# Optimization experiments

Hardware: AMD Instinct MI355X
Metric: run time of the kernel (lower is better)

The kernel has to match this reference:

```python
import jax, jax.numpy as jnp
import numpy as np
from jax.ops import segment_sum, segment_max

N = 50000      # nodes
E = 600000     # edges
D_IN = 128     # input_dim
H = 128        # hidden_dim
OUT = 32       # output_dim (classes)
G = 50         # graphs in batch
HEADS = 2


def setup_inputs() -> dict:
    key = jax.random.key(0)
    ks = jax.random.split(key, 16)
    s = 0.05
    inp = {
        "x": jax.random.normal(ks[0], (N, D_IN), jnp.float32),
        "edge_index": jax.random.randint(ks[1], (2, E), 0, N, dtype=jnp.int64),
        "batch": jnp.sort(jax.random.randint(ks[2], (N,), 0, G, dtype=jnp.int64)),
        # GCN layers: weight [in, out] (applied as x @ W), bias [out]
        "W1": jax.random.normal(ks[3], (D_IN, H), jnp.float32) * s,
        "b1": jnp.zeros((H,), jnp.float32),
        "W2": jax.random.normal(ks[4], (H, H), jnp.float32) * s,
        "b2": jnp.zeros((H,), jnp.float32),
        "W3": jax.random.normal(ks[5], (H, H), jnp.float32) * s,
        "b3": jnp.zeros((H,), jnp.float32),
        # GAT: lin weight [H, HEADS*H], attention vecs [HEADS, H], bias [H] (concat=False)
        "gat_W": jax.random.normal(ks[6], (H, HEADS * H), jnp.float32) * s,
        "att_src": jax.random.normal(ks[7], (HEADS, H), jnp.float32) * s,
        "att_dst": jax.random.normal(ks[8], (HEADS, H), jnp.float32) * s,
        "gat_b": jnp.zeros((H,), jnp.float32),
        # MLP head
        "fc1_W": jax.random.normal(ks[9], (H, H), jnp.float32) * s,
        "fc1_b": jnp.zeros((H,), jnp.float32),
        "fc2_W": jax.random.normal(ks[10], (H, OUT), jnp.float32) * s,
        "fc2_b": jnp.zeros((OUT,), jnp.float32),
    }
    return inp


def _add_self_loops(src, dst, n):
    loop = jnp.arange(n, dtype=src.dtype)
    return jnp.concatenate([src, loop]), jnp.concatenate([dst, loop])


def _gcn_conv(x, W, b, src, dst, n):
    # PyG GCNConv: self-loops + symmetric normalization deg^-1/2 A deg^-1/2
    h = x @ W                                  # [N, H]
    deg = segment_sum(jnp.ones_like(dst, dtype=h.dtype), dst, num_segments=n)
    dinv = jnp.where(deg > 0, jax.lax.rsqrt(deg), 0.0)
    norm = dinv[src] * dinv[dst]               # [E']
    out = segment_sum(h[src] * norm[:, None], dst, num_segments=n)
    return out + b


def _gat_conv(x, W, a_src, a_dst, b, src, dst, n):
    # PyG GATConv, heads=HEADS, concat=False (mean over heads), self-loops added
    h = (x @ W).reshape(n, HEADS, -1)          # [N, heads, H]
    al_s = jnp.einsum('nhc,hc->nh', h, a_src)  # [N, heads]
    al_d = jnp.einsum('nhc,hc->nh', h, a_dst)
    alpha = jax.nn.leaky_relu(al_s[src] + al_d[dst], 0.2)   # [E', heads]
    m = segment_max(alpha, dst, num_segments=n)             # per-dst max
    ea = jnp.exp(alpha - m[dst])
    denom = segment_sum(ea, dst, num_segments=n)
    coef = ea / (denom[dst] + 1e-16)                         # [E', heads]
    out = segment_sum(h[src] * coef[:, :, None], dst, num_segments=n)  # [N, heads, H]
    return out.mean(axis=1) + b


def reference(x, edge_index, batch, W1, b1, W2, b2, W3, b3,
              gat_W, att_src, att_dst, gat_b, fc1_W, fc1_b, fc2_W, fc2_b):
    n = x.shape[0]
    src, dst = _add_self_loops(edge_index[0], edge_index[1], n)
    h = jax.nn.relu(_gcn_conv(x, W1, b1, src, dst, n))
    h = jax.nn.relu(_gcn_conv(h, W2, b2, src, dst, n))
    h = jax.nn.relu(_gcn_conv(h, W3, b3, src, dst, n))
    h = jax.nn.relu(_gat_conv(h, gat_W, att_src, att_dst, gat_b, src, dst, n))
    # pooling: mean + add share the same segment sum
    sums = segment_sum(h, batch, num_segments=G)             # [G, H]
    counts = segment_sum(jnp.ones((n,), h.dtype), batch, num_segments=G)
    g = sums / jnp.maximum(counts, 1.0)[:, None] + sums
    g = jax.nn.relu(g @ fc1_W + fc1_b)
    logits = g @ fc2_W + fc2_b
    return jax.nn.log_softmax(logits, axis=1)
```

## Files before the change

### kernel.cpp

```cpp
#include <hip/hip_runtime.h>
#include <hip/hip_bf16.h>

typedef __attribute__((ext_vector_type(8))) short short8v;
typedef __attribute__((ext_vector_type(4))) float float4v;

__device__ __forceinline__ unsigned short f2bf(float f) {
    unsigned u = __float_as_uint(f);
    u += 0x7FFFu + ((u >> 16) & 1u);
    return (unsigned short)(u >> 16);
}
__device__ __forceinline__ float bflo(unsigned u) { return __uint_as_float(u << 16); }
__device__ __forceinline__ float bfhi(unsigned u) { return __uint_as_float(u & 0xFFFF0000u); }
__device__ __forceinline__ float lrelu02(float a) { return (a > 0.f) ? a : 0.2f * a; }
__device__ __forceinline__ unsigned pack2(float a, float b) {
    return (unsigned)f2bf(a) | ((unsigned)f2bf(b) << 16);
}


__global__ void deg_kernel(const int* __restrict__ dst, int* __restrict__ deg, int E) {
    int i = blockIdx.x * blockDim.x + threadIdx.x;
    if (i < E) atomicAdd(&deg[dst[i]], 1);
}

__global__ void dinv_kernel(const int* __restrict__ deg, float* __restrict__ dinv, int N) {
    int i = blockIdx.x * blockDim.x + threadIdx.x;
    if (i < N) dinv[i] = rsqrtf((float)(deg[i] + 1));
}

__global__ __launch_bounds__(1024) void scan_kernel(const int* __restrict__ deg,
                                                    int* __restrict__ ptr,
                                                    int* __restrict__ cursor, int N) {
    __shared__ int wsum[16];
    const int tid = threadIdx.x, wid = tid >> 6, lane = tid & 63;
    int carry = 0;
    for (int base = 0; base < N; base += 1024) {
        int i = base + tid;
        int v = (i < N) ? deg[i] : 0;
        int x = v;
#pragma unroll
        for (int o = 1; o < 64; o <<= 1) {
            int t = __shfl_up(x, o);
            if (lane >= o) x += t;
        }
        if (lane == 63) wsum[wid] = x;
        __syncthreads();
        if (wid == 0 && lane < 16) {
            int w = wsum[lane];
#pragma unroll
            for (int o = 1; o < 16; o <<= 1) {
                int t = __shfl_up(w, o);
                if (lane >= o) w += t;
            }
            wsum[lane] = w;
        }
        __syncthreads();
        int excl = carry + (wid ? wsum[wid - 1] : 0) + x - v;
        if (i < N) { ptr[i] = excl; cursor[i] = excl; }
        carry += wsum[15];
        __syncthreads();
    }
    if (tid == 0) ptr[N] = carry;
}

__global__ void csr_fill_kernel(const int* __restrict__ src, const int* __restrict__ dst,
                                int* __restrict__ cursor, int* __restrict__ csr_src, int E) {
    int e = blockIdx.x * blockDim.x + threadIdx.x;
    if (e < E) {
        int pos = atomicAdd(&cursor[dst[e]], 1);
        csr_src[pos] = src[e];
    }
}

__global__ void wt_conv_all_kernel(const float* __restrict__ W1, const float* __restrict__ W2,
                                   const float* __restrict__ W3, const float* __restrict__ WG,
                                   unsigned short* __restrict__ Wt1, unsigned short* __restrict__ Wt2,
                                   unsigned short* __restrict__ Wt3, unsigned short* __restrict__ WtG) {
    int idx = blockIdx.x * blockDim.x + threadIdx.x;
    if (idx < 16384) {
        int i = idx;           int k = i >> 7, n = i & 127;  Wt1[n * 128 + k] = f2bf(W1[i]);
    } else if (idx < 32768) {
        int i = idx - 16384;   int k = i >> 7, n = i & 127;  Wt2[n * 128 + k] = f2bf(W2[i]);
    } else if (idx < 49152) {
        int i = idx - 32768;   int k = i >> 7, n = i & 127;  Wt3[n * 128 + k] = f2bf(W3[i]);
    } else if (idx < 81920) {
        int i = idx - 49152;   int k = i >> 8, n = i & 255;  WtG[n * 128 + k] = f2bf(WG[i]);
    }
}

template<bool XF32>
__global__ __launch_bounds__(256) void lin_mfma_kernel(const void* __restrict__ Xv,
                                                       const unsigned short* __restrict__ Wt,
                                                       const float* __restrict__ dinv,
                                                       unsigned short* __restrict__ Y, int N) {
    constexpr int NF = 8;
    int wave = threadIdx.x >> 6;
    int lane = threadIdx.x & 63;
    int lr = lane & 15;
    int hk = lane >> 4;
    int rowbase = blockIdx.x * 64 + wave * 16;
    int arow = rowbase + lr; if (arow > N - 1) arow = N - 1;
    float4v acc[NF];
#pragma unroll
    for (int i = 0; i < NF; ++i) acc[i] = (float4v){0.f, 0.f, 0.f, 0.f};
#pragma unroll
    for (int ks = 0; ks < 4; ++ks) {
        int k0 = ks * 32 + hk * 8;
        short8v a;
        if (XF32) {
            const float* xp = (const float*)Xv + (size_t)arow * 128 + k0;
            float4 a0 = *(const float4*)xp;
            float4 a1 = *(const float4*)(xp + 4);
            a[0] = (short)f2bf(a0.x); a[1] = (short)f2bf(a0.y);
            a[2] = (short)f2bf(a0.z); a[3] = (short)f2bf(a0.w);
            a[4] = (short)f2bf(a1.x); a[5] = (short)f2bf(a1.y);
            a[6] = (short)f2bf(a1.z); a[7] = (short)f2bf(a1.w);
        } else {
            a = *(const short8v*)((const unsigned short*)Xv + (size_t)arow * 128 + k0);
        }
#pragma unroll
        for (int nf = 0; nf < NF; ++nf) {
            short8v b = *(const short8v*)(Wt + (size_t)(nf * 16 + lr) * 128 + k0);
            acc[nf] = __builtin_amdgcn_mfma_f32_16x16x32_bf16(a, b, acc[nf], 0, 0, 0);
        }
    }
#pragma unroll
    for (int r = 0; r < 4; ++r) {
        int orow = rowbase + hk * 4 + r;
        if (orow < N) {
            float scale = dinv[orow];
            unsigned short* yp = Y + (size_t)orow * 128 + lr;
#pragma unroll
            for (int nf = 0; nf < NF; ++nf) yp[nf * 16] = f2bf(acc[nf][r] * scale);
        }
    }
}

__global__ __launch_bounds__(256) void lin_mfma_attn_kernel(const unsigned short* __restrict__ X,
                                                            const unsigned short* __restrict__ Wt,
                                                            const float* __restrict__ attS,
                                                            const float* __restrict__ attD,
                                                            unsigned short* __restrict__ Y,
                                                            float2* __restrict__ al_s2,
                                                            float2* __restrict__ al_d2, int N) {
    constexpr int NF = 16;
    int wave = threadIdx.x >> 6;
    int lane = threadIdx.x & 63;
    int lr = lane & 15;
    int hk = lane >> 4;
    int rowbase = blockIdx.x * 64 + wave * 16;
    int arow = rowbase + lr; if (arow > N - 1) arow = N - 1;
    float4v acc[NF];
#pragma unroll
    for (int i = 0; i < NF; ++i) acc[i] = (float4v){0.f, 0.f, 0.f, 0.f};
#pragma unroll
    for (int ks = 0; ks < 4; ++ks) {
        int k0 = ks * 32 + hk * 8;
        short8v a = *(const short8v*)(X + (size_t)arow * 128 + k0);
#pragma unroll
        for (int nf = 0; nf < NF; ++nf) {
            short8v b = *(const short8v*)(Wt + (size_t)(nf * 16 + lr) * 128 + k0);
            acc[nf] = __builtin_amdgcn_mfma_f32_16x16x32_bf16(a, b, acc[nf], 0, 0, 0);
        }
    }
    float as0[8], as1[8], ad0[8], ad1[8];
#pragma unroll
    for (int q = 0; q < 8; ++q) {
        as0[q] = attS[q * 16 + lr];
        as1[q] = attS[128 + q * 16 + lr];
        ad0[q] = attD[q * 16 + lr];
        ad1[q] = attD[128 + q * 16 + lr];
    }
#pragma unroll
    for (int r = 0; r < 4; ++r) {
        int orow = rowbase + hk * 4 + r;
        float s0 = 0.f, s1 = 0.f, d0 = 0.f, d1 = 0.f;
#pragma unroll
        for (int q = 0; q < 8; ++q) {
            s0 += acc[q][r] * as0[q];
            d0 += acc[q][r] * ad0[q];
            s1 += acc[q + 8][r] * as1[q];
            d1 += acc[q + 8][r] * ad1[q];
        }
#pragma unroll
        for (int o = 1; o < 16; o <<= 1) {
            s0 += __shfl_xor(s0, o);
            s1 += __shfl_xor(s1, o);
            d0 += __shfl_xor(d0, o);
            d1 += __shfl_xor(d1, o);
        }
        if (orow < N) {
            unsigned short* yp = Y + (size_t)orow * 256 + lr;
#pragma unroll
            for (int nf = 0; nf < NF; ++nf) yp[nf * 16] = f2bf(acc[nf][r]);
            if (lr == 0) {
                al_s2[orow] = make_float2(s0, s1);
                al_d2[orow] = make_float2(d0, d1);
            }
        }
    }
}

__global__ __launch_bounds__(256) void gcn_gather_kernel(const uint4* __restrict__ y,
                                                         const float* __restrict__ dinv,
                                                         const int* __restrict__ ptr,
                                                         const int* __restrict__ csr,
                                                         const float* __restrict__ bias,
                                                         uint4* __restrict__ out, int N) {
    __shared__ int stg[4][64];
    int w = threadIdx.x >> 6;
    int node = blockIdx.x * 4 + w;
    if (node >= N) return;
    int lane = threadIdx.x & 63;
    int q = lane & 15;
    int g = lane >> 4;
    float a0 = 0.f, a1 = 0.f, a2 = 0.f, a3 = 0.f, a4 = 0.f, a5 = 0.f, a6 = 0.f, a7 = 0.f;
    int b0 = ptr[node], b1 = ptr[node + 1];
    for (int p0 = b0; p0 < b1; p0 += 64) {
        int m = b1 - p0; if (m > 64) m = 64;
        if (lane < m) stg[w][lane] = __builtin_nontemporal_load(csr + p0 + lane);
        int j = g;
        for (; j + 4 < m; j += 8) {
            int s0 = stg[w][j], s1 = stg[w][j + 4];
            uint4 u0 = y[(size_t)s0 * 16 + q];
            uint4 u1 = y[(size_t)s1 * 16 + q];
            a0 += bflo(u0.x) + bflo(u1.x); a1 += bfhi(u0.x) + bfhi(u1.x);
            a2 += bflo(u0.y) + bflo(u1.y); a3 += bfhi(u0.y) + bfhi(u1.y);
            a4 += bflo(u0.z) + bflo(u1.z); a5 += bfhi(u0.z) + bfhi(u1.z);
            a6 += bflo(u0.w) + bflo(u1.w); a7 += bfhi(u0.w) + bfhi(u1.w);
        }
        if (j < m) {
            int s0 = stg[w][j];
            uint4 u0 = y[(size_t)s0 * 16 + q];
            a0 += bflo(u0.x); a1 += bfhi(u0.x);
            a2 += bflo(u0.y); a3 += bfhi(u0.y);
            a4 += bflo(u0.z); a5 += bfhi(u0.z);
            a6 += bflo(u0.w); a7 += bfhi(u0.w);
        }
    }
#pragma unroll
    for (int o = 16; o < 64; o <<= 1) {
        a0 += __shfl_xor(a0, o); a1 += __shfl_xor(a1, o);
        a2 += __shfl_xor(a2, o); a3 += __shfl_xor(a3, o);
        a4 += __shfl_xor(a4, o); a5 += __shfl_xor(a5, o);
        a6 += __shfl_xor(a6, o); a7 += __shfl_xor(a7, o);
    }
    uint4 su = y[(size_t)node * 16 + q];
    a0 += bflo(su.x); a1 += bfhi(su.x);
    a2 += bflo(su.y); a3 += bfhi(su.y);
    a4 += bflo(su.z); a5 += bfhi(su.z);
    a6 += bflo(su.w); a7 += bfhi(su.w);
    if (lane < 16) {
        float dn = dinv[node];
        float4 bb0 = *(const float4*)(bias + q * 8);
        float4 bb1 = *(const float4*)(bias + q * 8 + 4);
        a0 = fmaxf(a0 * dn + bb0.x, 0.f); a1 = fmaxf(a1 * dn + bb0.y, 0.f);
        a2 = fmaxf(a2 * dn + bb0.z, 0.f); a3 = fmaxf(a3 * dn + bb0.w, 0.f);
        a4 = fmaxf(a4 * dn + bb1.x, 0.f); a5 = fmaxf(a5 * dn + bb1.y, 0.f);
        a6 = fmaxf(a6 * dn + bb1.z, 0.f); a7 = fmaxf(a7 * dn + bb1.w, 0.f);
        out[(size_t)node * 16 + q] = make_uint4(pack2(a0, a1), pack2(a2, a3),
                                                pack2(a4, a5), pack2(a6, a7));
    }
}

__global__ __launch_bounds__(256) void gat_gather_kernel(const uint4* __restrict__ h2,
                                                         const float2* __restrict__ al_s2,
                                                         const float2* __restrict__ al_d2,
                                                         const int* __restrict__ ptr,
                                                         const int* __restrict__ csr,
                                                         const float* __restrict__ bias,
                                                         uint4* __restrict__ out, int N) {
    __shared__ uint4 stg[4][64];
    int w = threadIdx.x >> 6;
    int node = blockIdx.x * 4 + w;
    if (node >= N) return;
    int lane = threadIdx.x & 63;
    int li = lane & 31;
    int head = li >> 4;
    int g = lane >> 5;
    int b0 = ptr[node], b1 = ptr[node + 1];
    float2 ad = al_d2[node];

    float den0 = 0.f, den1 = 0.f;
    float a0 = 0.f, a1 = 0.f, a2 = 0.f, a3 = 0.f, a4 = 0.f, a5 = 0.f, a6 = 0.f, a7 = 0.f;

    for (int p0 = b0; p0 < b1; p0 += 64) {
        int m = b1 - p0; if (m > 64) m = 64;
        int idx = (lane < m) ? __builtin_nontemporal_load(csr + p0 + lane) : 0;
        float2 als = al_s2[idx];
        float e0 = __expf(lrelu02(als.x + ad.x));
        float e1 = __expf(lrelu02(als.y + ad.y));
        if (lane >= m) { e0 = 0.f; e1 = 0.f; }
        den0 += e0; den1 += e1;
        stg[w][lane] = make_uint4((unsigned)idx, __float_as_uint(e0), __float_as_uint(e1), 0u);
        int j = g;
        for (; j + 2 < m; j += 4) {
            uint4 t0 = stg[w][j], t1 = stg[w][j + 2];
            uint4 u0 = h2[(size_t)t0.x * 32 + li];
            uint4 u1 = h2[(size_t)t1.x * 32 + li];
            float c0 = __uint_as_float(head ? t0.z : t0.y);
            float c1 = __uint_as_float(head ? t1.z : t1.y);
            a0 += bflo(u0.x) * c0 + bflo(u1.x) * c1; a1 += bfhi(u0.x) * c0 + bfhi(u1.x) * c1;
            a2 += bflo(u0.y) * c0 + bflo(u1.y) * c1; a3 += bfhi(u0.y) * c0 + bfhi(u1.y) * c1;
            a4 += bflo(u0.z) * c0 + bflo(u1.z) * c1; a5 += bfhi(u0.z) * c0 + bfhi(u1.z) * c1;
            a6 += bflo(u0.w) * c0 + bflo(u1.w) * c1; a7 += bfhi(u0.w) * c0 + bfhi(u1.w) * c1;
        }
        if (j < m) {
            uint4 t0 = stg[w][j];
            uint4 u0 = h2[(size_t)t0.x * 32 + li];
            float c0 = __uint_as_float(head ? t0.z : t0.y);
            a0 += bflo(u0.x) * c0; a1 += bfhi(u0.x) * c0;
            a2 += bflo(u0.y) * c0; a3 += bfhi(u0.y) * c0;
            a4 += bflo(u0.z) * c0; a5 += bfhi(u0.z) * c0;
            a6 += bflo(u0.w) * c0; a7 += bfhi(u0.w) * c0;
        }
    }
    a0 += __shfl_xor(a0, 32); a1 += __shfl_xor(a1, 32);
    a2 += __shfl_xor(a2, 32); a3 += __shfl_xor(a3, 32);
    a4 += __shfl_xor(a4, 32); a5 += __shfl_xor(a5, 32);
    a6 += __shfl_xor(a6, 32); a7 += __shfl_xor(a7, 32);
#pragma unroll
    for (int o = 1; o < 64; o <<= 1) {
        den0 += __shfl_xor(den0, o);
        den1 += __shfl_xor(den1, o);
    }
    {
        float2 as_ = al_s2[node];
        float e0s = __expf(lrelu02(as_.x + ad.x));
        float e1s = __expf(lrelu02(as_.y + ad.y));
        den0 += e0s; den1 += e1s;
        float ea = head ? e1s : e0s;
        uint4 u = h2[(size_t)node * 32 + li];
        a0 += ea * bflo(u.x); a1 += ea * bfhi(u.x);
        a2 += ea * bflo(u.y); a3 += ea * bfhi(u.y);
        a4 += ea * bflo(u.z); a5 += ea * bfhi(u.z);
        a6 += ea * bflo(u.w); a7 += ea * bfhi(u.w);
    }
    float inv = 1.f / ((head ? den1 : den0) + 1e-16f);
    a0 *= inv; a1 *= inv; a2 *= inv; a3 *= inv;
    a4 *= inv; a5 *= inv; a6 *= inv; a7 *= inv;
    a0 += __shfl_xor(a0, 16); a1 += __shfl_xor(a1, 16);
    a2 += __shfl_xor(a2, 16); a3 += __shfl_xor(a3, 16);
    a4 += __shfl_xor(a4, 16); a5 += __shfl_xor(a5, 16);
    a6 += __shfl_xor(a6, 16); a7 += __shfl_xor(a7, 16);
    if (lane < 16) {
        int q = lane;
        float4 bb0 = *(const float4*)(bias + q * 8);
        float4 bb1 = *(const float4*)(bias + q * 8 + 4);
        a0 = fmaxf(0.5f * a0 + bb0.x, 0.f); a1 = fmaxf(0.5f * a1 + bb0.y, 0.f);
        a2 = fmaxf(0.5f * a2 + bb0.z, 0.f); a3 = fmaxf(0.5f * a3 + bb0.w, 0.f);
        a4 = fmaxf(0.5f * a4 + bb1.x, 0.f); a5 = fmaxf(0.5f * a5 + bb1.y, 0.f);
        a6 = fmaxf(0.5f * a6 + bb1.z, 0.f); a7 = fmaxf(0.5f * a7 + bb1.w, 0.f);
        out[(size_t)node * 16 + q] = make_uint4(pack2(a0, a1), pack2(a2, a3),
                                                pack2(a4, a5), pack2(a6, a7));
    }
}

__global__ __launch_bounds__(256) void pool_kernel(const unsigned* __restrict__ h,
                                                   const int* __restrict__ batch,
                                                   float* __restrict__ sums,
                                                   float* __restrict__ counts, int N) {
    const int PER = 32;
    int wave = threadIdx.x >> 6;
    int f = threadIdx.x & 63;
    int n0 = (blockIdx.x * 4 + wave) * PER;
    int n1 = min(N, n0 + PER);
    if (n0 >= n1) return;
    int cur = -1;
    float a0 = 0.f, a1 = 0.f, cnt = 0.f;
    for (int n = n0; n < n1; ++n) {
        int g = batch[n];
        if (g != cur) {
            if (cur >= 0) {
                atomicAdd(&sums[cur * 128 + f * 2], a0);
                atomicAdd(&sums[cur * 128 + f * 2 + 1], a1);
                if (f == 0) atomicAdd(&counts[cur], cnt);
            }
            cur = g; a0 = a1 = cnt = 0.f;
        }
        unsigned u = h[(size_t)n * 64 + f];
        a0 += bflo(u); a1 += bfhi(u); cnt += 1.f;
    }
    if (cur >= 0) {
        atomicAdd(&sums[cur * 128 + f * 2], a0);
        atomicAdd(&sums[cur * 128 + f * 2 + 1], a1);
        if (f == 0) atomicAdd(&counts[cur], cnt);
    }
}

__global__ __launch_bounds__(128) void head_kernel(const float* __restrict__ sums,
                                                   const float* __restrict__ counts,
                                                   const float* __restrict__ fc1W,
                                                   const float* __restrict__ fc1b,
                                                   const float* __restrict__ fc2W,
                                                   const float* __restrict__ fc2b,
                                                   float* __restrict__ out) {
    int g = blockIdx.x;
    int tid = threadIdx.x;
    __shared__ float gm[128];
    __shared__ float h1[128];
    __shared__ float part[4][32];
    float s = sums[g * 128 + tid];
    gm[tid] = s / fmaxf(counts[g], 1.f) + s;
    __syncthreads();
    float acc = fc1b[tid];
    for (int k = 0; k < 128; ++k) acc += gm[k] * fc1W[k * 128 + tid];
    h1[tid] = fmaxf(acc, 0.f);
    __syncthreads();
    int c = tid & 31, p = tid >> 5;
    float a2 = 0.f;
    for (int k = p * 32; k < p * 32 + 32; ++k) a2 += h1[k] * fc2W[k * 32 + c];
    part[p][c] = a2;
    __syncthreads();
    if (tid < 32) {
        float v = part[0][tid] + part[1][tid] + part[2][tid] + part[3][tid] + fc2b[tid];
        float m = v;
#pragma unroll
        for (int o = 1; o < 32; o <<= 1) m = fmaxf(m, __shfl_xor(m, o));
        float e = __expf(v - m);
        float ssum = e;
#pragma unroll
        for (int o = 1; o < 32; o <<= 1) ssum += __shfl_xor(ssum, o);
        out[g * 32 + tid] = v - m - logf(ssum);
    }
}


extern "C" void kernel_launch(void* const* d_in, const int* in_sizes, int n_in,
                              void* d_out, int out_size, void* d_ws, size_t ws_size,
                              hipStream_t stream) {
    const float* x     = (const float*)d_in[0];
    const int*   eidx  = (const int*)d_in[1];
    const int*   batch = (const int*)d_in[2];
    const float* W1 = (const float*)d_in[3];
    const float* b1 = (const float*)d_in[4];
    const float* W2 = (const float*)d_in[5];
    const float* b2 = (const float*)d_in[6];
    const float* W3 = (const float*)d_in[7];
    const float* b3 = (const float*)d_in[8];
    const float* gatW   = (const float*)d_in[9];
    const float* attSrc = (const float*)d_in[10];
    const float* attDst = (const float*)d_in[11];
    const float* gatB   = (const float*)d_in[12];
    const float* fc1W = (const float*)d_in[13];
    const float* fc1b = (const float*)d_in[14];
    const float* fc2W = (const float*)d_in[15];
    const float* fc2b = (const float*)d_in[16];
    float* out = (float*)d_out;

    const int N  = in_sizes[0] / 128;
    const int E  = in_sizes[1] / 2;
    const int OUT = in_sizes[15] / 128;
    const int G   = out_size / OUT;

    const int* src = eidx;
    const int* dst = eidx + E;

    char* ws = (char*)d_ws;
    size_t off = 0;
    auto carve = [&](size_t bytes) { char* p = ws + off; off += (bytes + 255) & ~255ull; return p; };
    unsigned short* yb   = (unsigned short*)carve((size_t)N * 128 * 2);
    unsigned short* hb   = (unsigned short*)carve((size_t)N * 128 * 2);
    unsigned short* gb   = (unsigned short*)carve((size_t)N * 256 * 2);
    unsigned short* Wt1 = (unsigned short*)carve(128 * 128 * 2);
    unsigned short* Wt2 = (unsigned short*)carve(128 * 128 * 2);
    unsigned short* Wt3 = (unsigned short*)carve(128 * 128 * 2);
    unsigned short* WtG = (unsigned short*)carve(256 * 128 * 2);
    int*   deg   = (int*)carve((size_t)N * 4);
    float* dinv  = (float*)carve((size_t)N * 4);
    int*   ptr   = (int*)carve((size_t)(N + 1) * 4);
    int*   cursor= (int*)carve((size_t)N * 4);
    int*   csrS  = (int*)carve((size_t)E * 4);
    float* al_s  = (float*)carve((size_t)N * 2 * 4);
    float* al_d  = (float*)carve((size_t)N * 2 * 4);
    float* sums  = (float*)carve((size_t)G * 128 * 4);
    float* cnts  = (float*)carve((size_t)G * 4);

    const int B = 256;
    dim3 blk(B);
    auto cdiv = [](long long a, long long b) { return (int)((a + b - 1) / b); };

    wt_conv_all_kernel<<<cdiv(81920, B), blk, 0, stream>>>(W1, W2, W3, gatW, Wt1, Wt2, Wt3, WtG);

    hipMemsetAsync(deg, 0, (size_t)N * 4, stream);
    deg_kernel<<<cdiv(E, B), blk, 0, stream>>>(dst, deg, E);
    dinv_kernel<<<cdiv(N, B), blk, 0, stream>>>(deg, dinv, N);
    scan_kernel<<<1, 1024, 0, stream>>>(deg, ptr, cursor, N);
    csr_fill_kernel<<<cdiv(E, B), blk, 0, stream>>>(src, dst, cursor, csrS, E);

    lin_mfma_kernel<true><<<cdiv(N, 64), blk, 0, stream>>>(x, Wt1, dinv, yb, N);
    gcn_gather_kernel<<<cdiv(N, 4), blk, 0, stream>>>((const uint4*)yb, dinv, ptr, csrS, b1, (uint4*)hb, N);
    lin_mfma_kernel<false><<<cdiv(N, 64), blk, 0, stream>>>(hb, Wt2, dinv, yb, N);
    gcn_gather_kernel<<<cdiv(N, 4), blk, 0, stream>>>((const uint4*)yb, dinv, ptr, csrS, b2, (uint4*)hb, N);
    lin_mfma_kernel<false><<<cdiv(N, 64), blk, 0, stream>>>(hb, Wt3, dinv, yb, N);
    gcn_gather_kernel<<<cdiv(N, 4), blk, 0, stream>>>((const uint4*)yb, dinv, ptr, csrS, b3, (uint4*)hb, N);

    lin_mfma_attn_kernel<<<cdiv(N, 64), blk, 0, stream>>>(hb, WtG, attSrc, attDst, gb,
                                                          (float2*)al_s, (float2*)al_d, N);
    gat_gather_kernel<<<cdiv(N, 4), blk, 0, stream>>>((const uint4*)gb, (const float2*)al_s, (const float2*)al_d,
                                                      ptr, csrS, gatB, (uint4*)yb, N);

    hipMemsetAsync(sums, 0, (size_t)G * 128 * 4, stream);
    hipMemsetAsync(cnts, 0, (size_t)G * 4, stream);
    pool_kernel<<<cdiv(N, 128), blk, 0, stream>>>((const unsigned*)yb, batch, sums, cnts, N);

    head_kernel<<<G, dim3(128), 0, stream>>>(sums, cnts, fc1W, fc1b, fc2W, fc2b, out);
}
```

Measured before the change: 391.0 us.

## Store GAT features in fp8, fuse setup memsets and dinv into kernels

The GAT linear output is now stored as packed fp8 instead of bf16, which halves the bytes gathered per edge in the attention aggregation. The gather kernel unpacks the fp8 values and uses shared memory to undo the permuted column layout before applying bias and ReLU. Separately, the weight conversion and the zeroing of deg, sums and counts are merged into one setup kernel, and dinv is computed inside the scan kernel, removing several launches and memsets. fp8 storage lowers the precision of the GAT features and risks accuracy loss.

```diff
diff --git a/kernel.cpp b/kernel.cpp
--- a/kernel.cpp
+++ b/kernel.cpp
@@ -3,6 +3,7 @@
 
 typedef __attribute__((ext_vector_type(8))) short short8v;
 typedef __attribute__((ext_vector_type(4))) float float4v;
+typedef __attribute__((ext_vector_type(2))) float f32x2;
 
 __device__ __forceinline__ unsigned short f2bf(float f) {
     unsigned u = __float_as_uint(f);
@@ -16,65 +17,12 @@
     return (unsigned)f2bf(a) | ((unsigned)f2bf(b) << 16);
 }
 
-
-__global__ void deg_kernel(const int* __restrict__ dst, int* __restrict__ deg, int E) {
-    int i = blockIdx.x * blockDim.x + threadIdx.x;
-    if (i < E) atomicAdd(&deg[dst[i]], 1);
-}
-
-__global__ void dinv_kernel(const int* __restrict__ deg, float* __restrict__ dinv, int N) {
-    int i = blockIdx.x * blockDim.x + threadIdx.x;
-    if (i < N) dinv[i] = rsqrtf((float)(deg[i] + 1));
-}
-
-__global__ __launch_bounds__(1024) void scan_kernel(const int* __restrict__ deg,
-                                                    int* __restrict__ ptr,
-                                                    int* __restrict__ cursor, int N) {
-    __shared__ int wsum[16];
-    const int tid = threadIdx.x, wid = tid >> 6, lane = tid & 63;
-    int carry = 0;
-    for (int base = 0; base < N; base += 1024) {
-        int i = base + tid;
-        int v = (i < N) ? deg[i] : 0;
-        int x = v;
-#pragma unroll
-        for (int o = 1; o < 64; o <<= 1) {
-            int t = __shfl_up(x, o);
-            if (lane >= o) x += t;
-        }
-        if (lane == 63) wsum[wid] = x;
-        __syncthreads();
-        if (wid == 0 && lane < 16) {
-            int w = wsum[lane];
-#pragma unroll
-            for (int o = 1; o < 16; o <<= 1) {
-                int t = __shfl_up(w, o);
-                if (lane >= o) w += t;
-            }
-            wsum[lane] = w;
-        }
-        __syncthreads();
-        int excl = carry + (wid ? wsum[wid - 1] : 0) + x - v;
-        if (i < N) { ptr[i] = excl; cursor[i] = excl; }
-        carry += wsum[15];
-        __syncthreads();
-    }
-    if (tid == 0) ptr[N] = carry;
-}
-
-__global__ void csr_fill_kernel(const int* __restrict__ src, const int* __restrict__ dst,
-                                int* __restrict__ cursor, int* __restrict__ csr_src, int E) {
-    int e = blockIdx.x * blockDim.x + threadIdx.x;
-    if (e < E) {
-        int pos = atomicAdd(&cursor[dst[e]], 1);
-        csr_src[pos] = src[e];
-    }
-}
-
-__global__ void wt_conv_all_kernel(const float* __restrict__ W1, const float* __restrict__ W2,
-                                   const float* __restrict__ W3, const float* __restrict__ WG,
-                                   unsigned short* __restrict__ Wt1, unsigned short* __restrict__ Wt2,
-                                   unsigned short* __restrict__ Wt3, unsigned short* __restrict__ WtG) {
+__global__ void setup_kernel(const float* __restrict__ W1, const float* __restrict__ W2,
+                             const float* __restrict__ W3, const float* __restrict__ WG,
+                             unsigned short* __restrict__ Wt1, unsigned short* __restrict__ Wt2,
+                             unsigned short* __restrict__ Wt3, unsigned short* __restrict__ WtG,
+                             int* __restrict__ deg, float* __restrict__ sums,
+                             float* __restrict__ cnts, int N, int G) {
     int idx = blockIdx.x * blockDim.x + threadIdx.x;
     if (idx < 16384) {
         int i = idx;           int k = i >> 7, n = i & 127;  Wt1[n * 128 + k] = f2bf(W1[i]);
@@ -84,6 +32,66 @@
         int i = idx - 32768;   int k = i >> 7, n = i & 127;  Wt3[n * 128 + k] = f2bf(W3[i]);
     } else if (idx < 81920) {
         int i = idx - 49152;   int k = i >> 8, n = i & 255;  WtG[n * 128 + k] = f2bf(WG[i]);
+    } else if (idx < 81920 + N) {
+        deg[idx - 81920] = 0;
+    } else if (idx < 81920 + N + G * 128) {
+        sums[idx - 81920 - N] = 0.f;
+    } else if (idx < 81920 + N + G * 128 + G) {
+        cnts[idx - 81920 - N - G * 128] = 0.f;
+    }
+}
+
+
+__global__ void deg_kernel(const int* __restrict__ dst, int* __restrict__ deg, int E) {
+    int i = blockIdx.x * blockDim.x + threadIdx.x;
+    if (i < E) atomicAdd(&deg[dst[i]], 1);
+}
+
+__global__ __launch_bounds__(1024) void scan_kernel(const int* __restrict__ deg,
+                                                    int* __restrict__ ptr,
+                                                    int* __restrict__ cursor,
+                                                    float* __restrict__ dinv, int N) {
+    __shared__ int wsum[16];
+    const int tid = threadIdx.x, wid = tid >> 6, lane = tid & 63;
+    int carry = 0;
+    for (int base = 0; base < N; base += 1024) {
+        int i = base + tid;
+        int v = (i < N) ? deg[i] : 0;
+        int x = v;
+#pragma unroll
+        for (int o = 1; o < 64; o <<= 1) {
+            int t = __shfl_up(x, o);
+            if (lane >= o) x += t;
+        }
+        if (lane == 63) wsum[wid] = x;
+        __syncthreads();
+        if (wid == 0 && lane < 16) {
+            int w = wsum[lane];
+#pragma unroll
+            for (int o = 1; o < 16; o <<= 1) {
+                int t = __shfl_up(w, o);
+                if (lane >= o) w += t;
+            }
+            wsum[lane] = w;
+        }
+        __syncthreads();
+        int excl = carry + (wid ? wsum[wid - 1] : 0) + x - v;
+        if (i < N) {
+            ptr[i] = excl; cursor[i] = excl;
+            dinv[i] = rsqrtf((float)v + 1.0f);
+        }
+        carry += wsum[15];
+        __syncthreads();
+    }
+    if (tid == 0) ptr[N] = carry;
+}
+
+__global__ void csr_fill_kernel(const int* __restrict__ src, const int* __restrict__ dst,
+                                int* __restrict__ cursor, int* __restrict__ csr_src, int E) {
+    int e = blockIdx.x * blockDim.x + threadIdx.x;
+    if (e < E) {
+        int pos = atomicAdd(&cursor[dst[e]], 1);
+        csr_src[pos] = src[e];
     }
 }
 
@@ -139,7 +147,7 @@
                                                             const unsigned short* __restrict__ Wt,
                                                             const float* __restrict__ attS,
                                                             const float* __restrict__ attD,
-                                                            unsigned short* __restrict__ Y,
+                                                            uint2* __restrict__ Yf8,
                                                             float2* __restrict__ al_s2,
                                                             float2* __restrict__ al_d2, int N) {
     constexpr int NF = 16;
@@ -189,9 +197,16 @@
             d1 += __shfl_xor(d1, o);
         }
         if (orow < N) {
-            unsigned short* yp = Y + (size_t)orow * 256 + lr;
-#pragma unroll
-            for (int nf = 0; nf < NF; ++nf) yp[nf * 16] = f2bf(acc[nf][r]);
+            int w0 = __builtin_amdgcn_cvt_pk_fp8_f32(acc[0][r], acc[1][r], 0, 0);
+            w0 = __builtin_amdgcn_cvt_pk_fp8_f32(acc[2][r], acc[3][r], w0, 1);
+            int w1 = __builtin_amdgcn_cvt_pk_fp8_f32(acc[4][r], acc[5][r], 0, 0);
+            w1 = __builtin_amdgcn_cvt_pk_fp8_f32(acc[6][r], acc[7][r], w1, 1);
+            Yf8[(size_t)orow * 32 + lr] = make_uint2((unsigned)w0, (unsigned)w1);
+            int w2 = __builtin_amdgcn_cvt_pk_fp8_f32(acc[8][r], acc[9][r], 0, 0);
+            w2 = __builtin_amdgcn_cvt_pk_fp8_f32(acc[10][r], acc[11][r], w2, 1);
+            int w3 = __builtin_amdgcn_cvt_pk_fp8_f32(acc[12][r], acc[13][r], 0, 0);
+            w3 = __builtin_amdgcn_cvt_pk_fp8_f32(acc[14][r], acc[15][r], w3, 1);
+            Yf8[(size_t)orow * 32 + 16 + lr] = make_uint2((unsigned)w2, (unsigned)w3);
             if (lr == 0) {
                 al_s2[orow] = make_float2(s0, s1);
                 al_d2[orow] = make_float2(d0, d1);
@@ -262,7 +277,7 @@
     }
 }
 
-__global__ __launch_bounds__(256) void gat_gather_kernel(const uint4* __restrict__ h2,
+__global__ __launch_bounds__(256) void gat_gather_kernel(const uint2* __restrict__ h2,
                                                          const float2* __restrict__ al_s2,
                                                          const float2* __restrict__ al_d2,
                                                          const int* __restrict__ ptr,
@@ -270,6 +285,7 @@
                                                          const float* __restrict__ bias,
                                                          uint4* __restrict__ out, int N) {
     __shared__ uint4 stg[4][64];
+    __shared__ float vals[4][128];
     int w = threadIdx.x >> 6;
     int node = blockIdx.x * 4 + w;
     if (node >= N) return;
@@ -295,23 +311,35 @@
         int j = g;
         for (; j + 2 < m; j += 4) {
             uint4 t0 = stg[w][j], t1 = stg[w][j + 2];
-            uint4 u0 = h2[(size_t)t0.x * 32 + li];
-            uint4 u1 = h2[(size_t)t1.x * 32 + li];
+            uint2 u0 = h2[(size_t)t0.x * 32 + li];
+            uint2 u1 = h2[(size_t)t1.x * 32 + li];
             float c0 = __uint_as_float(head ? t0.z : t0.y);
             float c1 = __uint_as_float(head ? t1.z : t1.y);
-            a0 += bflo(u0.x) * c0 + bflo(u1.x) * c1; a1 += bfhi(u0.x) * c0 + bfhi(u1.x) * c1;
-            a2 += bflo(u0.y) * c0 + bflo(u1.y) * c1; a3 += bfhi(u0.y) * c0 + bfhi(u1.y) * c1;
-            a4 += bflo(u0.z) * c0 + bflo(u1.z) * c1; a5 += bfhi(u0.z) * c0 + bfhi(u1.z) * c1;
-            a6 += bflo(u0.w) * c0 + bflo(u1.w) * c1; a7 += bfhi(u0.w) * c0 + bfhi(u1.w) * c1;
+            f32x2 p0v = __builtin_amdgcn_cvt_pk_f32_fp8(u0.x, 0);
+            f32x2 p1v = __builtin_amdgcn_cvt_pk_f32_fp8(u0.x, 1);
+            f32x2 p2v = __builtin_amdgcn_cvt_pk_f32_fp8(u0.y, 0);
+            f32x2 p3v = __builtin_amdgcn_cvt_pk_f32_fp8(u0.y, 1);
+            f32x2 q0v = __builtin_amdgcn_cvt_pk_f32_fp8(u1.x, 0);
+            f32x2 q1v = __builtin_amdgcn_cvt_pk_f32_fp8(u1.x, 1);
+            f32x2 q2v = __builtin_amdgcn_cvt_pk_f32_fp8(u1.y, 0);
+            f32x2 q3v = __builtin_amdgcn_cvt_pk_f32_fp8(u1.y, 1);
+            a0 += p0v[0] * c0 + q0v[0] * c1; a1 += p0v[1] * c0 + q0v[1] * c1;
+            a2 += p1v[0] * c0 + q1v[0] * c1; a3 += p1v[1] * c0 + q1v[1] * c1;
+            a4 += p2v[0] * c0 + q2v[0] * c1; a5 += p2v[1] * c0 + q2v[1] * c1;
+            a6 += p3v[0] * c0 + q3v[0] * c1; a7 += p3v[1] * c0 + q3v[1] * c1;
         }
         if (j < m) {
             uint4 t0 = stg[w][j];
-            uint4 u0 = h2[(size_t)t0.x * 32 + li];
+            uint2 u0 = h2[(size_t)t0.x * 32 + li];
             float c0 = __uint_as_float(head ? t0.z : t0.y);
-            a0 += bflo(u0.x) * c0; a1 += bfhi(u0.x) * c0;
-            a2 += bflo(u0.y) * c0; a3 += bfhi(u0.y) * c0;
-            a4 += bflo(u0.z) * c0; a5 += bfhi(u0.z) * c0;
-            a6 += bflo(u0.w) * c0; a7 += bfhi(u0.w) * c0;
+            f32x2 p0v = __builtin_amdgcn_cvt_pk_f32_fp8(u0.x, 0);
+            f32x2 p1v = __builtin_amdgcn_cvt_pk_f32_fp8(u0.x, 1);
+            f32x2 p2v = __builtin_amdgcn_cvt_pk_f32_fp8(u0.y, 0);
+            f32x2 p3v = __builtin_amdgcn_cvt_pk_f32_fp8(u0.y, 1);
+            a0 += p0v[0] * c0; a1 += p0v[1] * c0;
+            a2 += p1v[0] * c0; a3 += p1v[1] * c0;
+            a4 += p2v[0] * c0; a5 += p2v[1] * c0;
+            a6 += p3v[0] * c0; a7 += p3v[1] * c0;
         }
     }
     a0 += __shfl_xor(a0, 32); a1 += __shfl_xor(a1, 32);
@@ -329,11 +357,15 @@
         float e1s = __expf(lrelu02(as_.y + ad.y));
         den0 += e0s; den1 += e1s;
         float ea = head ? e1s : e0s;
-        uint4 u = h2[(size_t)node * 32 + li];
-        a0 += ea * bflo(u.x); a1 += ea * bfhi(u.x);
-        a2 += ea * bflo(u.y); a3 += ea * bfhi(u.y);
-        a4 += ea * bflo(u.z); a5 += ea * bfhi(u.z);
-        a6 += ea * bflo(u.w); a7 += ea * bfhi(u.w);
+        uint2 u = h2[(size_t)node * 32 + li];
+        f32x2 p0v = __builtin_amdgcn_cvt_pk_f32_fp8(u.x, 0);
+        f32x2 p1v = __builtin_amdgcn_cvt_pk_f32_fp8(u.x, 1);
+        f32x2 p2v = __builtin_amdgcn_cvt_pk_f32_fp8(u.y, 0);
+        f32x2 p3v = __builtin_amdgcn_cvt_pk_f32_fp8(u.y, 1);
+        a0 += ea * p0v[0]; a1 += ea * p0v[1];
+        a2 += ea * p1v[0]; a3 += ea * p1v[1];
+        a4 += ea * p2v[0]; a5 += ea * p2v[1];
+        a6 += ea * p3v[0]; a7 += ea * p3v[1];
     }
     float inv = 1.f / ((head ? den1 : den0) + 1e-16f);
     a0 *= inv; a1 *= inv; a2 *= inv; a3 *= inv;
@@ -343,15 +375,21 @@
     a4 += __shfl_xor(a4, 16); a5 += __shfl_xor(a5, 16);
     a6 += __shfl_xor(a6, 16); a7 += __shfl_xor(a7, 16);
     if (lane < 16) {
-        int q = lane;
-        float4 bb0 = *(const float4*)(bias + q * 8);
-        float4 bb1 = *(const float4*)(bias + q * 8 + 4);
-        a0 = fmaxf(0.5f * a0 + bb0.x, 0.f); a1 = fmaxf(0.5f * a1 + bb0.y, 0.f);
-        a2 = fmaxf(0.5f * a2 + bb0.z, 0.f); a3 = fmaxf(0.5f * a3 + bb0.w, 0.f);
-        a4 = fmaxf(0.5f * a4 + bb1.x, 0.f); a5 = fmaxf(0.5f * a5 + bb1.y, 0.f);
-        a6 = fmaxf(0.5f * a6 + bb1.z, 0.f); a7 = fmaxf(0.5f * a7 + bb1.w, 0.f);
-        out[(size_t)node * 16 + q] = make_uint4(pack2(a0, a1), pack2(a2, a3),
-                                                pack2(a4, a5), pack2(a6, a7));
+        vals[w][lane * 8 + 0] = a0; vals[w][lane * 8 + 1] = a1;
+        vals[w][lane * 8 + 2] = a2; vals[w][lane * 8 + 3] = a3;
+        vals[w][lane * 8 + 4] = a4; vals[w][lane * 8 + 5] = a5;
+        vals[w][lane * 8 + 6] = a6; vals[w][lane * 8 + 7] = a7;
+    }
+    if (lane < 16) {
+        float o[8];
+#pragma unroll
+        for (int i = 0; i < 8; ++i) {
+            int c = lane * 8 + i;
+            int p = (c & 15) * 8 + (c >> 4);
+            o[i] = fmaxf(0.5f * vals[w][p] + bias[c], 0.f);
+        }
+        out[(size_t)node * 16 + lane] = make_uint4(pack2(o[0], o[1]), pack2(o[2], o[3]),
+                                                   pack2(o[4], o[5]), pack2(o[6], o[7]));
     }
 }
 
@@ -460,7 +498,7 @@
     auto carve = [&](size_t bytes) { char* p = ws + off; off += (bytes + 255) & ~255ull; return p; };
     unsigned short* yb   = (unsigned short*)carve((size_t)N * 128 * 2);
     unsigned short* hb   = (unsigned short*)carve((size_t)N * 128 * 2);
-    unsigned short* gb   = (unsigned short*)carve((size_t)N * 256 * 2);
+    uint2*          gb8  = (uint2*)carve((size_t)N * 256);
     unsigned short* Wt1 = (unsigned short*)carve(128 * 128 * 2);
     unsigned short* Wt2 = (unsigned short*)carve(128 * 128 * 2);
     unsigned short* Wt3 = (unsigned short*)carve(128 * 128 * 2);
@@ -479,12 +517,11 @@
     dim3 blk(B);
     auto cdiv = [](long long a, long long b) { return (int)((a + b - 1) / b); };
 
-    wt_conv_all_kernel<<<cdiv(81920, B), blk, 0, stream>>>(W1, W2, W3, gatW, Wt1, Wt2, Wt3, WtG);
-
-    hipMemsetAsync(deg, 0, (size_t)N * 4, stream);
+    setup_kernel<<<cdiv(81920 + N + G * 128 + G, B), blk, 0, stream>>>(
+        W1, W2, W3, gatW, Wt1, Wt2, Wt3, WtG, deg, sums, cnts, N, G);
+
     deg_kernel<<<cdiv(E, B), blk, 0, stream>>>(dst, deg, E);
-    dinv_kernel<<<cdiv(N, B), blk, 0, stream>>>(deg, dinv, N);
-    scan_kernel<<<1, 1024, 0, stream>>>(deg, ptr, cursor, N);
+    scan_kernel<<<1, 1024, 0, stream>>>(deg, ptr, cursor, dinv, N);
     csr_fill_kernel<<<cdiv(E, B), blk, 0, stream>>>(src, dst, cursor, csrS, E);
 
     lin_mfma_kernel<true><<<cdiv(N, 64), blk, 0, stream>>>(x, Wt1, dinv, yb, N);
@@ -494,13 +531,11 @@
     lin_mfma_kernel<false><<<cdiv(N, 64), blk, 0, stream>>>(hb, Wt3, dinv, yb, N);
     gcn_gather_kernel<<<cdiv(N, 4), blk, 0, stream>>>((const uint4*)yb, dinv, ptr, csrS, b3, (uint4*)hb, N);
 
-    lin_mfma_attn_kernel<<<cdiv(N, 64), blk, 0, stream>>>(hb, WtG, attSrc, attDst, gb,
+    lin_mfma_attn_kernel<<<cdiv(N, 64), blk, 0, stream>>>(hb, WtG, attSrc, attDst, gb8,
                                                           (float2*)al_s, (float2*)al_d, N);
-    gat_gather_kernel<<<cdiv(N, 4), blk, 0, stream>>>((const uint4*)gb, (const float2*)al_s, (const float2*)al_d,
+    gat_gather_kernel<<<cdiv(N, 4), blk, 0, stream>>>(gb8, (const float2*)al_s, (const float2*)al_d,
                                                       ptr, csrS, gatB, (uint4*)yb, N);
 
-    hipMemsetAsync(sums, 0, (size_t)G * 128 * 4, stream);
-    hipMemsetAsync(cnts, 0, (size_t)G * 4, stream);
     pool_kernel<<<cdiv(N, 128), blk, 0, stream>>>((const unsigned*)yb, batch, sums, cnts, N);
 
     head_kernel<<<G, dim3(128), 0, stream>>>(sums, cnts, fc1W, fc1b, fc2W, fc2b, out);
```

After: 372.7 us. -4.7%, faster.
